# Performance work log

Measured on AMD Instinct MI355X. Metric: run time of the kernel, lower is better.

Reference implementation:

```python
import jax, jax.numpy as jnp
import numpy as np

B, T, K, H = 4, 2048, 1024, 16
D = K // H

def setup_inputs() -> dict:
    key = jax.random.key(0)
    kx, kq, kk, kv = jax.random.split(key, 4)
    s = 1.0 / np.sqrt(K)
    return {
        "x": jax.random.normal(kx, (B, T, K), dtype=jnp.float32),
        "Wq": jax.random.normal(kq, (K, K), dtype=jnp.float32) * s,
        "Wk": jax.random.normal(kk, (K, K), dtype=jnp.float32) * s,
        "Wv": jax.random.normal(kv, (K, K), dtype=jnp.float32) * s,
    }

def reference(x, Wq, Wk, Wv):
    b, t, k = x.shape
    h, d = H, K // H
    # projections -> (b, h, t, d)
    q = (x @ Wq.T).reshape(b, t, h, d).transpose(0, 2, 1, 3)
    ke = (x @ Wk.T).reshape(b, t, h, d).transpose(0, 2, 1, 3)
    v = (x @ Wv.T).reshape(b, t, h, d).transpose(0, 2, 1, 3)
    scale = d ** (-0.25)  # applied to both q and k, as in the original
    scores = jnp.einsum('bhqd,bhkd->bhqk', q * scale, ke * scale)
    causal = jnp.triu(jnp.ones((t, t), dtype=bool), k=1)
    scores = jnp.where(causal, -jnp.inf, scores)
    attn = jax.nn.softmax(scores, axis=-1)
    out = jnp.einsum('bhqk,bhkd->bhqd', attn, v)
    return out.transpose(0, 2, 1, 3).reshape(b, t, k)
```

## Files before the change

kernel.cpp:

```cpp
#include <hip/hip_runtime.h>
#include <hip/hip_bf16.h>
#include <math.h>

#define B_   4
#define T_   2048
#define KDIM 1024
#define H_   16
#define D_   64
#define BH_  (B_*H_)
#define M_   (B_*T_)
#define NKT  (KDIM/64)

typedef __bf16 bf16;
typedef __bf16 bf16x8 __attribute__((ext_vector_type(8)));
typedef __bf16 bf16x4 __attribute__((ext_vector_type(4)));
typedef float  f32x4  __attribute__((ext_vector_type(4)));
typedef float  f32x16 __attribute__((ext_vector_type(16)));
typedef unsigned int u32;
typedef u32 u32x4 __attribute__((ext_vector_type(4)));

static __device__ __forceinline__ f32x4 mfma16(bf16x8 a, bf16x8 b, f32x4 c) {
    return __builtin_amdgcn_mfma_f32_16x16x32_bf16(a, b, c, 0, 0, 0);
}
static __device__ __forceinline__ f32x16 mfma32(bf16x8 a, bf16x8 b, f32x16 c) {
    return __builtin_amdgcn_mfma_f32_32x32x16_bf16(a, b, c, 0, 0, 0);
}
static __device__ __forceinline__ float exp2_fast(float x) {
    float r; asm("v_exp_f32 %0, %1" : "=v"(r) : "v"(x)); return r;
}

__global__ void cvt_all(const float* __restrict__ x,  const float* __restrict__ Wq,
                        const float* __restrict__ Wk, const float* __restrict__ Wv,
                        bf16* __restrict__ dst) {
    int i = blockIdx.x * blockDim.x + threadIdx.x;
    const int NX = M_*KDIM/4, NW = KDIM*KDIM/4;
    const float* src;
    int j;
    if (i < NX)                { src = x;  j = i; }
    else if (i < NX + NW)      { src = Wq; j = i - NX; }
    else if (i < NX + 2*NW)    { src = Wk; j = i - NX - NW; }
    else                       { src = Wv; j = i - NX - 2*NW; }
    float4 v = reinterpret_cast<const float4*>(src)[j];
    bf16x4 o;
    o.x = (bf16)v.x; o.y = (bf16)v.y; o.z = (bf16)v.z; o.w = (bf16)v.w;
    reinterpret_cast<bf16x4*>(dst)[i] = o;
}

__global__ __launch_bounds__(512) void proj_gemm256(
    const bf16* __restrict__ xb, const bf16* __restrict__ Wflat,
    bf16* __restrict__ Qb, bf16* __restrict__ Kb, bf16* __restrict__ Vtb)
{
    __shared__ __align__(16) char As[3*32768];
    __shared__ __align__(16) char Bs[3*16384];

    const int tid  = threadIdx.x;
    const int wid  = tid >> 6;
    const int lane = tid & 63;
    const int l15  = lane & 15, l4 = lane >> 4;
    const int wavem = wid >> 1, waven = wid & 1;

    const int orig = blockIdx.x;
    const int xcd  = orig & 7;
    const int idx  = orig >> 3;
    const int mblk = xcd * 4 + (idx & 3);
    const int nblk = idx >> 2;
    const int row0 = mblk * 256, col0 = nblk * 128;

    const bf16* asrc[4];
#pragma unroll
    for (int q = 0; q < 4; ++q) {
        int c   = q*512 + tid;
        int rr  = c >> 3;
        int cb  = (c & 7) * 16;
        int cbs = cb ^ ((rr & 7) << 4);
        asrc[q] = xb + (size_t)(row0 + rr)*KDIM + (cbs >> 1);
    }
    const bf16* bsrc[2];
#pragma unroll
    for (int q = 0; q < 2; ++q) {
        int c   = q*512 + tid;
        int rr  = c >> 3;
        int cb  = (c & 7) * 16;
        int cbs = cb ^ ((rr & 7) << 4);
        bsrc[q] = Wflat + (size_t)(col0 + rr)*KDIM + (cbs >> 1);
    }

    auto stage = [&](int kt, int buf) {
        const int k0 = kt * 64;
        char* Ab = As + buf*32768;
        char* Bb = Bs + buf*16384;
#pragma unroll
        for (int q = 0; q < 4; ++q) {
            char* la = Ab + (q*512 + wid*64)*16;
            __builtin_amdgcn_global_load_lds(
                (const __attribute__((address_space(1))) void*)(asrc[q] + k0),
                (__attribute__((address_space(3))) void*)la, 16, 0, 0);
        }
#pragma unroll
        for (int q = 0; q < 2; ++q) {
            char* lb = Bb + (q*512 + wid*64)*16;
            __builtin_amdgcn_global_load_lds(
                (const __attribute__((address_space(1))) void*)(bsrc[q] + k0),
                (__attribute__((address_space(3))) void*)lb, 16, 0, 0);
        }
    };

    f32x4 acc[4][4] = {};

    const int sw    = (l15 & 7) << 4;
    const int arow  = (wavem*64 + l15) * 128;
    const int brow  = (waven*64 + l15) * 128;

    stage(0, 0);
    stage(1, 1);
    asm volatile("s_waitcnt vmcnt(6)" ::: "memory");
    __builtin_amdgcn_sched_barrier(0);
    __builtin_amdgcn_s_barrier();

#pragma unroll
    for (int t = 0; t < NKT; ++t) {
        const int bt = t % 3;
        const int b2 = (t + 2) % 3;
        if (t + 2 < NKT) stage(t + 2, b2);

        const char* Ap = As + bt*32768;
        const char* Bp = Bs + bt*16384;
        bf16x8 af[2][4], bfr[2][4];
#pragma unroll
        for (int kk = 0; kk < 2; ++kk) {
            const int cbk = (kk*64 + l4*16) ^ sw;
#pragma unroll
            for (int m = 0; m < 4; ++m)
                af[kk][m] = *reinterpret_cast<const bf16x8*>(Ap + arow + m*2048 + cbk);
#pragma unroll
            for (int n = 0; n < 4; ++n)
                bfr[kk][n] = *reinterpret_cast<const bf16x8*>(Bp + brow + n*2048 + cbk);
        }
        __builtin_amdgcn_s_setprio(1);
#pragma unroll
        for (int kk = 0; kk < 2; ++kk)
#pragma unroll
            for (int m = 0; m < 4; ++m)
#pragma unroll
                for (int n = 0; n < 4; ++n)
                    acc[m][n] = mfma16(af[kk][m], bfr[kk][n], acc[m][n]);
        __builtin_amdgcn_s_setprio(0);

        if (t < NKT - 1) {
            if (t + 2 < NKT) {
                asm volatile("s_waitcnt vmcnt(6)" ::: "memory");
            } else {
                asm volatile("s_waitcnt vmcnt(0)" ::: "memory");
            }
            __builtin_amdgcn_sched_barrier(0);
            __builtin_amdgcn_s_barrier();
        }
    }

#pragma unroll
    for (int m = 0; m < 4; ++m)
#pragma unroll
        for (int n = 0; n < 4; ++n)
#pragma unroll
            for (int r = 0; r < 4; ++r) {
                int gi = row0 + wavem*64 + m*16 + l4*4 + r;
                int gj = col0 + waven*64 + n*16 + l15;
                int wz  = gj >> 10;
                int gjw = gj & 1023;
                float v = acc[m][n][r];
                if (wz == 0) v *= 0.18033688011112042f;
                bf16 o = (bf16)v;
                int bb = gi >> 11, tt = gi & (T_-1);
                int hh = gjw >> 6, dd = gjw & (D_-1);
                size_t bh = (size_t)bb*H_ + hh;
                if (wz == 0)      Qb [(bh*T_ + tt)*D_ + dd] = o;
                else if (wz == 1) Kb [(bh*T_ + tt)*D_ + dd] = o;
                else              Vtb[(bh*D_ + dd)*T_ + tt] = o;
            }
}

__global__ __launch_bounds__(256) void flash_attn3(
    const bf16* __restrict__ Qb, const bf16* __restrict__ Kb,
    const bf16* __restrict__ Vtb, float* __restrict__ out)
{
    __shared__ __align__(16) char Ksm[8192];
    __shared__ __align__(16) char Vsm[8192];

    const int tid  = threadIdx.x;
    const int wid  = tid >> 6;
    const int lane = tid & 63;
    const int l31  = lane & 31;
    const int hi   = lane >> 5;

    const int orig = blockIdx.x;
    const int wg   = (orig & 7) * 128 + (orig >> 3);
    const int bh   = wg >> 4;
    const int qblk = (15 - (wg & 15)) * 128;
    const int q0   = qblk + wid * 32;
    const int q_abs = q0 + l31;

    const bf16* qp = Qb + ((size_t)bh*T_ + q_abs)*D_ + hi*8;
    bf16x8 qf[4];
#pragma unroll
    for (int j = 0; j < 4; ++j)
        qf[j] = *reinterpret_cast<const bf16x8*>(qp + j*16);

    const bf16* kbase = Kb  + (size_t)bh*T_*D_;
    const bf16* vbase = Vtb + (size_t)bh*D_*T_;

    f32x16 o0 = {}; f32x16 o1 = {};
    float lsum = 0.f;

    const int my_nt  = (q0 + 31) >> 6;
    const int blk_nt = qblk/64 + 1;
    const int tmaskb = q_abs - 4*hi;

    const int r0 = tid >> 3,          r1 = (tid + 256) >> 3;
    const int e0 = (tid & 7) * 8,     e1 = e0;
    const u32 lds0 = (u32)((r0*128 + e0*2) ^ ((r0 & 7) << 4));
    const u32 lds1 = (u32)((r1*128 + e1*2) ^ ((r1 & 7) << 4));

    u32x4 kr0, kr1, vr0, vr1;
    auto issue = [&](int nt) {
        kr0 = *reinterpret_cast<const u32x4*>(kbase + ((size_t)(nt*64 + r0))*D_ + e0);
        kr1 = *reinterpret_cast<const u32x4*>(kbase + ((size_t)(nt*64 + r1))*D_ + e1);
        vr0 = *reinterpret_cast<const u32x4*>(vbase + (size_t)r0*T_ + nt*64 + e0);
        vr1 = *reinterpret_cast<const u32x4*>(vbase + (size_t)r1*T_ + nt*64 + e1);
    };
    issue(0);

    auto subtile = [&](int s, int kvb_abs, bool maskit, bf16x8& pA, bf16x8& pB) {
        f32x16 sacc = {};
        const int row = s*32 + l31;
        const int swk = (row & 7) << 4;
#pragma unroll
        for (int j = 0; j < 4; ++j) {
            bf16x8 kf = *reinterpret_cast<const bf16x8*>(Ksm + ((row*128 + j*32 + hi*16) ^ swk));
            sacc = mfma32(kf, qf[j], sacc);
        }
        const int tlim = tmaskb - kvb_abs;
        float p[16];
#pragma unroll
        for (int r = 0; r < 16; ++r) {
            const int crow0 = (r & 3) + 8*(r >> 2);
            float sv = sacc[r];
            if (maskit) sv = (crow0 > tlim) ? -INFINITY : sv;
            p[r] = exp2_fast(sv);
        }
        {
            float a0 = p[0]+p[1],   a1 = p[2]+p[3],   a2 = p[4]+p[5],   a3 = p[6]+p[7];
            float a4 = p[8]+p[9],   a5 = p[10]+p[11], a6 = p[12]+p[13], a7 = p[14]+p[15];
            lsum += ((a0+a1) + (a2+a3)) + ((a4+a5) + (a6+a7));
        }
        u32 w[8];
#pragma unroll
        for (int i = 0; i < 8; ++i) {
            u32 wv;
            asm("v_cvt_pk_bf16_f32 %0, %1, %2" : "=v"(wv) : "v"(p[2*i]), "v"(p[2*i+1]));
            w[i] = wv;
        }
        u32 a0w = w[0], a2w = w[2];
        asm("v_permlane32_swap_b32 %0, %1" : "+v"(a0w), "+v"(a2w));
        u32 a1w = w[1], a3w = w[3];
        asm("v_permlane32_swap_b32 %0, %1" : "+v"(a1w), "+v"(a3w));
        u32 b0w = w[4], b2w = w[6];
        asm("v_permlane32_swap_b32 %0, %1" : "+v"(b0w), "+v"(b2w));
        u32 b1w = w[5], b3w = w[7];
        asm("v_permlane32_swap_b32 %0, %1" : "+v"(b1w), "+v"(b3w));
        u32x4 A0 = {a0w, a1w, a2w, a3w};
        u32x4 A1 = {b0w, b1w, b2w, b3w};
        pA = __builtin_bit_cast(bf16x8, A0);
        pB = __builtin_bit_cast(bf16x8, A1);
    };

    auto pv = [&](int ks, bf16x8 pf) {
        const int swv = (l31 & 7) << 4;
        const int colb = ks*32 + hi*16;
        bf16x8 v0 = *reinterpret_cast<const bf16x8*>(Vsm + ((l31*128 + colb) ^ swv));
        bf16x8 v1 = *reinterpret_cast<const bf16x8*>(Vsm + (((32 + l31)*128 + colb) ^ swv));
        o0 = mfma32(v0, pf, o0);
        o1 = mfma32(v1, pf, o1);
    };

    for (int nt = 0; nt <= blk_nt; ++nt) {
        __syncthreads();
        *reinterpret_cast<u32x4*>(Ksm + lds0) = kr0;
        *reinterpret_cast<u32x4*>(Ksm + lds1) = kr1;
        *reinterpret_cast<u32x4*>(Vsm + lds0) = vr0;
        *reinterpret_cast<u32x4*>(Vsm + lds1) = vr1;
        __syncthreads();
        if (nt < blk_nt) issue(nt + 1);

        if (nt <= my_nt) {
            const bool partial = (nt == my_nt);
            const int  nsub = (!partial || (q0 & 32)) ? 2 : 1;
            bf16x8 pA, pB;
            subtile(0, nt*64, partial, pA, pB);
            pv(0, pA);
            pv(1, pB);
            if (nsub == 2) {
                subtile(1, nt*64 + 32, partial, pA, pB);
                pv(2, pA);
                pv(3, pB);
            }
        }
    }

    lsum += __shfl_xor(lsum, 32);
    const float inv = 1.0f / lsum;
    const int bb = bh >> 4, hh = bh & 15;
    float* orow = out + ((size_t)bb*T_ + q_abs)*KDIM + hh*64 + hi*4;
#pragma unroll
    for (int g = 0; g < 4; ++g) {
        f32x4 v0, v1;
#pragma unroll
        for (int j = 0; j < 4; ++j) { v0[j] = o0[g*4+j]*inv; v1[j] = o1[g*4+j]*inv; }
        *reinterpret_cast<f32x4*>(orow + g*8)      = v0;
        *reinterpret_cast<f32x4*>(orow + 32 + g*8) = v1;
    }
}

extern "C" void kernel_launch(void* const* d_in, const int* in_sizes, int n_in,
                              void* d_out, int out_size, void* d_ws, size_t ws_size,
                              hipStream_t stream) {
    (void)in_sizes; (void)n_in; (void)out_size; (void)ws_size;
    const float* x  = (const float*)d_in[0];
    const float* Wq = (const float*)d_in[1];
    const float* Wk = (const float*)d_in[2];
    const float* Wv = (const float*)d_in[3];
    float* out = (float*)d_out;

    bf16* xb  = (bf16*)d_ws;
    bf16* Wb  = xb + (size_t)M_*KDIM;
    bf16* Qb  = Wb + (size_t)3*KDIM*KDIM;
    bf16* Kb  = Qb + (size_t)M_*KDIM;
    bf16* Vtb = Kb + (size_t)M_*KDIM;

    const int n4 = (M_*KDIM + 3*KDIM*KDIM) / 4;
    cvt_all<<<(n4 + 255)/256, 256, 0, stream>>>(x, Wq, Wk, Wv, xb);

    proj_gemm256<<<dim3(768), 512, 0, stream>>>(xb, Wb, Qb, Kb, Vtb);
    flash_attn3<<<dim3(BH_*16), 256, 0, stream>>>(Qb, Kb, Vtb, out);
}
```

Baseline: 153.6 us.

## Enlarge projection GEMM tile to 256x256 with four-phase interleaved loads

The QKV projection GEMM moves from a 256x128 tile with a triple-buffered stage to a 256x256 tile with double buffering. Each k-step is split into four compute phases, and the global-to-LDS loads for the next k-tile are spread across those phases with explicit barriers and waitcnts. The intent is more arithmetic per byte loaded and better overlap of loads with MFMA work. In exchange, the grid halves to 384 blocks on 256 CUs, which leaves some CUs with a second wave of blocks. It also doubles the accumulator registers and adds more barriers per k-step.

```diff
diff --git a/kernel.cpp b/kernel.cpp
--- a/kernel.cpp
+++ b/kernel.cpp
@@ -46,125 +46,120 @@
     reinterpret_cast<bf16x4*>(dst)[i] = o;
 }
 
-__global__ __launch_bounds__(512) void proj_gemm256(
+__global__ __launch_bounds__(512) void proj_gemm8p(
     const bf16* __restrict__ xb, const bf16* __restrict__ Wflat,
     bf16* __restrict__ Qb, bf16* __restrict__ Kb, bf16* __restrict__ Vtb)
 {
-    __shared__ __align__(16) char As[3*32768];
-    __shared__ __align__(16) char Bs[3*16384];
+    __shared__ __align__(16) char As[2*32768];
+    __shared__ __align__(16) char Bs[2*32768];
 
     const int tid  = threadIdx.x;
     const int wid  = tid >> 6;
     const int lane = tid & 63;
     const int l15  = lane & 15, l4 = lane >> 4;
-    const int wavem = wid >> 1, waven = wid & 1;
+    const int wm   = wid >> 2;
+    const int wn   = wid & 3;
 
     const int orig = blockIdx.x;
     const int xcd  = orig & 7;
     const int idx  = orig >> 3;
     const int mblk = xcd * 4 + (idx & 3);
     const int nblk = idx >> 2;
-    const int row0 = mblk * 256, col0 = nblk * 128;
-
-    const bf16* asrc[4];
-#pragma unroll
-    for (int q = 0; q < 4; ++q) {
-        int c   = q*512 + tid;
-        int rr  = c >> 3;
-        int cb  = (c & 7) * 16;
-        int cbs = cb ^ ((rr & 7) << 4);
-        asrc[q] = xb + (size_t)(row0 + rr)*KDIM + (cbs >> 1);
+    const int row0 = mblk * 256, col0 = nblk * 256;
+
+    const int srow  = tid >> 3;
+    const int scolb = (tid & 7) * 16;
+    const int scbs  = scolb ^ ((srow & 7) << 4);
+    const bf16* aS[4]; const bf16* bS[4];
+#pragma unroll
+    for (int c = 0; c < 4; ++c) {
+        aS[c] = xb    + (size_t)(row0 + c*64 + srow)*KDIM + (scbs >> 1);
+        bS[c] = Wflat + (size_t)(col0 + c*64 + srow)*KDIM + (scbs >> 1);
     }
-    const bf16* bsrc[2];
-#pragma unroll
-    for (int q = 0; q < 2; ++q) {
-        int c   = q*512 + tid;
-        int rr  = c >> 3;
-        int cb  = (c & 7) * 16;
-        int cbs = cb ^ ((rr & 7) << 4);
-        bsrc[q] = Wflat + (size_t)(col0 + rr)*KDIM + (cbs >> 1);
-    }
-
-    auto stage = [&](int kt, int buf) {
-        const int k0 = kt * 64;
-        char* Ab = As + buf*32768;
-        char* Bb = Bs + buf*16384;
-#pragma unroll
-        for (int q = 0; q < 4; ++q) {
-            char* la = Ab + (q*512 + wid*64)*16;
-            __builtin_amdgcn_global_load_lds(
-                (const __attribute__((address_space(1))) void*)(asrc[q] + k0),
-                (__attribute__((address_space(3))) void*)la, 16, 0, 0);
-        }
-#pragma unroll
-        for (int q = 0; q < 2; ++q) {
-            char* lb = Bb + (q*512 + wid*64)*16;
-            __builtin_amdgcn_global_load_lds(
-                (const __attribute__((address_space(1))) void*)(bsrc[q] + k0),
-                (__attribute__((address_space(3))) void*)lb, 16, 0, 0);
-        }
-    };
-
-    f32x4 acc[4][4] = {};
-
-    const int sw    = (l15 & 7) << 4;
-    const int arow  = (wavem*64 + l15) * 128;
-    const int brow  = (waven*64 + l15) * 128;
-
-    stage(0, 0);
-    stage(1, 1);
-    asm volatile("s_waitcnt vmcnt(6)" ::: "memory");
+
+    auto stA = [&](int kt, int c) {
+        if (kt >= NKT) return;
+        char* d = As + ((kt & 1)*32768 + c*8192 + wid*1024);
+        __builtin_amdgcn_global_load_lds(
+            (const __attribute__((address_space(1))) void*)(aS[c] + kt*64),
+            (__attribute__((address_space(3))) void*)d, 16, 0, 0);
+    };
+    auto stB = [&](int kt, int c) {
+        if (kt >= NKT) return;
+        char* d = Bs + ((kt & 1)*32768 + c*8192 + wid*1024);
+        __builtin_amdgcn_global_load_lds(
+            (const __attribute__((address_space(1))) void*)(bS[c] + kt*64),
+            (__attribute__((address_space(3))) void*)d, 16, 0, 0);
+    };
+
+    f32x4 acc[8][4] = {};
+    const int sw = (l15 & 7) << 4;
+
+#define PHASE(MQ, NQ, STAGES, WAITS) do {                                              \
+    bf16x8 af_[2][4]; bf16x8 bf_[2][2];                                                \
+    _Pragma("unroll")                                                                  \
+    for (int kk = 0; kk < 2; ++kk) {                                                   \
+        const int cbk = (kk*64 + l4*16) ^ sw;                                          \
+        _Pragma("unroll")                                                              \
+        for (int m = 0; m < 4; ++m)                                                    \
+            af_[kk][m] = *reinterpret_cast<const bf16x8*>(                             \
+                Ap + (wm*128 + (MQ)*64 + m*16 + l15)*128 + cbk);                       \
+        _Pragma("unroll")                                                              \
+        for (int n = 0; n < 2; ++n)                                                    \
+            bf_[kk][n] = *reinterpret_cast<const bf16x8*>(                             \
+                Bp + (wn*64 + (NQ)*32 + n*16 + l15)*128 + cbk);                        \
+    }                                                                                  \
+    STAGES;                                                                            \
+    WAITS;                                                                             \
+    __builtin_amdgcn_s_barrier();                                                      \
+    __builtin_amdgcn_sched_barrier(0);                                                 \
+    asm volatile("s_waitcnt lgkmcnt(0)" ::: "memory");                                 \
+    __builtin_amdgcn_sched_barrier(0);                                                 \
+    __builtin_amdgcn_s_setprio(1);                                                     \
+    _Pragma("unroll")                                                                  \
+    for (int kk = 0; kk < 2; ++kk)                                                     \
+        _Pragma("unroll")                                                              \
+        for (int m = 0; m < 4; ++m)                                                    \
+            _Pragma("unroll")                                                          \
+            for (int n = 0; n < 2; ++n)                                                \
+                acc[(MQ)*4+m][(NQ)*2+n] =                                              \
+                    mfma16(af_[kk][m], bf_[kk][n], acc[(MQ)*4+m][(NQ)*2+n]);           \
+    __builtin_amdgcn_s_setprio(0);                                                     \
+    __builtin_amdgcn_s_barrier();                                                      \
+    __builtin_amdgcn_sched_barrier(0);                                                 \
+} while (0)
+
+#pragma unroll
+    for (int c = 0; c < 4; ++c) { stA(0, c); stB(0, c); }
+    asm volatile("s_waitcnt vmcnt(0)" ::: "memory");
     __builtin_amdgcn_sched_barrier(0);
     __builtin_amdgcn_s_barrier();
 
-#pragma unroll
     for (int t = 0; t < NKT; ++t) {
-        const int bt = t % 3;
-        const int b2 = (t + 2) % 3;
-        if (t + 2 < NKT) stage(t + 2, b2);
-
-        const char* Ap = As + bt*32768;
-        const char* Bp = Bs + bt*16384;
-        bf16x8 af[2][4], bfr[2][4];
-#pragma unroll
-        for (int kk = 0; kk < 2; ++kk) {
-            const int cbk = (kk*64 + l4*16) ^ sw;
-#pragma unroll
-            for (int m = 0; m < 4; ++m)
-                af[kk][m] = *reinterpret_cast<const bf16x8*>(Ap + arow + m*2048 + cbk);
-#pragma unroll
-            for (int n = 0; n < 4; ++n)
-                bfr[kk][n] = *reinterpret_cast<const bf16x8*>(Bp + brow + n*2048 + cbk);
-        }
-        __builtin_amdgcn_s_setprio(1);
-#pragma unroll
-        for (int kk = 0; kk < 2; ++kk)
-#pragma unroll
-            for (int m = 0; m < 4; ++m)
-#pragma unroll
-                for (int n = 0; n < 4; ++n)
-                    acc[m][n] = mfma16(af[kk][m], bfr[kk][n], acc[m][n]);
-        __builtin_amdgcn_s_setprio(0);
-
-        if (t < NKT - 1) {
-            if (t + 2 < NKT) {
-                asm volatile("s_waitcnt vmcnt(6)" ::: "memory");
-            } else {
-                asm volatile("s_waitcnt vmcnt(0)" ::: "memory");
-            }
-            __builtin_amdgcn_sched_barrier(0);
-            __builtin_amdgcn_s_barrier();
-        }
+        const char* Ap = As + (t & 1)*32768;
+        const char* Bp = Bs + (t & 1)*32768;
+        const bool more = (t < NKT - 1);
+
+        PHASE(0, 0, { stA(t+1, 0); stA(t+1, 2); }, (void)0);
+        PHASE(0, 1, { stB(t+1, 0); stB(t+1, 1); },
+              { if (more) { asm volatile("s_waitcnt vmcnt(4)" ::: "memory"); }
+                else      { asm volatile("s_waitcnt vmcnt(0)" ::: "memory"); }
+                __builtin_amdgcn_sched_barrier(0); });
+        PHASE(1, 0, { stB(t+1, 2); stB(t+1, 3); }, (void)0);
+        PHASE(1, 1, { stA(t+1, 1); stA(t+1, 3); },
+              { if (more) { asm volatile("s_waitcnt vmcnt(2)" ::: "memory");
+                            __builtin_amdgcn_sched_barrier(0); } });
     }
-
-#pragma unroll
-    for (int m = 0; m < 4; ++m)
+#undef PHASE
+
+#pragma unroll
+    for (int m = 0; m < 8; ++m)
 #pragma unroll
         for (int n = 0; n < 4; ++n)
 #pragma unroll
             for (int r = 0; r < 4; ++r) {
-                int gi = row0 + wavem*64 + m*16 + l4*4 + r;
-                int gj = col0 + waven*64 + n*16 + l15;
+                int gi = row0 + wm*128 + m*16 + l4*4 + r;
+                int gj = col0 + wn*64  + n*16 + l15;
                 int wz  = gj >> 10;
                 int gjw = gj & 1023;
                 float v = acc[m][n][r];
@@ -216,16 +211,16 @@
     const int tmaskb = q_abs - 4*hi;
 
     const int r0 = tid >> 3,          r1 = (tid + 256) >> 3;
-    const int e0 = (tid & 7) * 8,     e1 = e0;
+    const int e0 = (tid & 7) * 8;
     const u32 lds0 = (u32)((r0*128 + e0*2) ^ ((r0 & 7) << 4));
-    const u32 lds1 = (u32)((r1*128 + e1*2) ^ ((r1 & 7) << 4));
+    const u32 lds1 = (u32)((r1*128 + e0*2) ^ ((r1 & 7) << 4));
 
     u32x4 kr0, kr1, vr0, vr1;
     auto issue = [&](int nt) {
         kr0 = *reinterpret_cast<const u32x4*>(kbase + ((size_t)(nt*64 + r0))*D_ + e0);
-        kr1 = *reinterpret_cast<const u32x4*>(kbase + ((size_t)(nt*64 + r1))*D_ + e1);
+        kr1 = *reinterpret_cast<const u32x4*>(kbase + ((size_t)(nt*64 + r1))*D_ + e0);
         vr0 = *reinterpret_cast<const u32x4*>(vbase + (size_t)r0*T_ + nt*64 + e0);
-        vr1 = *reinterpret_cast<const u32x4*>(vbase + (size_t)r1*T_ + nt*64 + e1);
+        vr1 = *reinterpret_cast<const u32x4*>(vbase + (size_t)r1*T_ + nt*64 + e0);
     };
     issue(0);
 
@@ -339,6 +334,6 @@
     const int n4 = (M_*KDIM + 3*KDIM*KDIM) / 4;
     cvt_all<<<(n4 + 255)/256, 256, 0, stream>>>(x, Wq, Wk, Wv, xb);
 
-    proj_gemm256<<<dim3(768), 512, 0, stream>>>(xb, Wb, Qb, Kb, Vtb);
+    proj_gemm8p<<<dim3(384), 512, 0, stream>>>(xb, Wb, Qb, Kb, Vtb);
     flash_attn3<<<dim3(BH_*16), 256, 0, stream>>>(Qb, Kb, Vtb, out);
 }
```

Measured after the change: 178.3 us. +16.1%, slower.

## Replace triple-buffered 256x128 projection GEMM with single-buffered 128x128 tiles

Applied to the files above, without the earlier changes.

The projection GEMM goes from 256x128 tiles with 512 threads and a three-stage LDS pipeline to 128x128 tiles with 256 threads and one LDS buffer, synchronised with syncthreads and a full vmcnt(0) wait each k-step. The grid doubles to 1536 blocks and LDS per block shrinks a lot, which could allow more resident blocks and hide latency through occupancy rather than software pipelining. The cost is that loads no longer overlap the MFMA work inside a block, each tile is reused less, and the priority hints are removed. The attention kernel only has a redundant variable removed.

```diff
diff --git a/kernel.cpp b/kernel.cpp
--- a/kernel.cpp
+++ b/kernel.cpp
@@ -46,114 +46,77 @@
     reinterpret_cast<bf16x4*>(dst)[i] = o;
 }
 
-__global__ __launch_bounds__(512) void proj_gemm256(
+__global__ __launch_bounds__(256) void proj_gemm97(
     const bf16* __restrict__ xb, const bf16* __restrict__ Wflat,
     bf16* __restrict__ Qb, bf16* __restrict__ Kb, bf16* __restrict__ Vtb)
 {
-    __shared__ __align__(16) char As[3*32768];
-    __shared__ __align__(16) char Bs[3*16384];
+    __shared__ __align__(16) char Asm[128*128];
+    __shared__ __align__(16) char Bsm[128*128];
 
     const int tid  = threadIdx.x;
     const int wid  = tid >> 6;
     const int lane = tid & 63;
     const int l15  = lane & 15, l4 = lane >> 4;
-    const int wavem = wid >> 1, waven = wid & 1;
+    const int wr = wid >> 1, wc = wid & 1;
 
     const int orig = blockIdx.x;
     const int xcd  = orig & 7;
     const int idx  = orig >> 3;
-    const int mblk = xcd * 4 + (idx & 3);
-    const int nblk = idx >> 2;
-    const int row0 = mblk * 256, col0 = nblk * 128;
-
-    const bf16* asrc[4];
+    const int mblk = xcd * 8 + (idx & 7);
+    const int nblk = idx >> 3;
+    const int row0 = mblk * 128, col0 = nblk * 128;
+
+    const bf16* aS[4]; const bf16* bS[4];
 #pragma unroll
     for (int q = 0; q < 4; ++q) {
-        int c   = q*512 + tid;
+        int c   = q*256 + tid;
         int rr  = c >> 3;
         int cb  = (c & 7) * 16;
         int cbs = cb ^ ((rr & 7) << 4);
-        asrc[q] = xb + (size_t)(row0 + rr)*KDIM + (cbs >> 1);
+        aS[q] = xb    + (size_t)(row0 + rr)*KDIM + (cbs >> 1);
+        bS[q] = Wflat + (size_t)(col0 + rr)*KDIM + (cbs >> 1);
     }
-    const bf16* bsrc[2];
-#pragma unroll
-    for (int q = 0; q < 2; ++q) {
-        int c   = q*512 + tid;
-        int rr  = c >> 3;
-        int cb  = (c & 7) * 16;
-        int cbs = cb ^ ((rr & 7) << 4);
-        bsrc[q] = Wflat + (size_t)(col0 + rr)*KDIM + (cbs >> 1);
-    }
-
-    auto stage = [&](int kt, int buf) {
+
+    f32x4 acc[4][4] = {};
+    const int sw   = (l15 & 7) << 4;
+    const int arow = (wr*64 + l15) * 128;
+    const int brow = (wc*64 + l15) * 128;
+
+    for (int kt = 0; kt < NKT; ++kt) {
         const int k0 = kt * 64;
-        char* Ab = As + buf*32768;
-        char* Bb = Bs + buf*16384;
+        __syncthreads();
 #pragma unroll
         for (int q = 0; q < 4; ++q) {
-            char* la = Ab + (q*512 + wid*64)*16;
+            char* la = Asm + (q*256 + wid*64)*16;
             __builtin_amdgcn_global_load_lds(
-                (const __attribute__((address_space(1))) void*)(asrc[q] + k0),
+                (const __attribute__((address_space(1))) void*)(aS[q] + k0),
                 (__attribute__((address_space(3))) void*)la, 16, 0, 0);
         }
 #pragma unroll
-        for (int q = 0; q < 2; ++q) {
-            char* lb = Bb + (q*512 + wid*64)*16;
+        for (int q = 0; q < 4; ++q) {
+            char* lb = Bsm + (q*256 + wid*64)*16;
             __builtin_amdgcn_global_load_lds(
-                (const __attribute__((address_space(1))) void*)(bsrc[q] + k0),
+                (const __attribute__((address_space(1))) void*)(bS[q] + k0),
                 (__attribute__((address_space(3))) void*)lb, 16, 0, 0);
         }
-    };
-
-    f32x4 acc[4][4] = {};
-
-    const int sw    = (l15 & 7) << 4;
-    const int arow  = (wavem*64 + l15) * 128;
-    const int brow  = (waven*64 + l15) * 128;
-
-    stage(0, 0);
-    stage(1, 1);
-    asm volatile("s_waitcnt vmcnt(6)" ::: "memory");
-    __builtin_amdgcn_sched_barrier(0);
-    __builtin_amdgcn_s_barrier();
-
-#pragma unroll
-    for (int t = 0; t < NKT; ++t) {
-        const int bt = t % 3;
-        const int b2 = (t + 2) % 3;
-        if (t + 2 < NKT) stage(t + 2, b2);
-
-        const char* Ap = As + bt*32768;
-        const char* Bp = Bs + bt*16384;
-        bf16x8 af[2][4], bfr[2][4];
+        asm volatile("s_waitcnt vmcnt(0)" ::: "memory");
+        __syncthreads();
+
 #pragma unroll
         for (int kk = 0; kk < 2; ++kk) {
             const int cbk = (kk*64 + l4*16) ^ sw;
+            bf16x8 af[4], bfr[4];
 #pragma unroll
             for (int m = 0; m < 4; ++m)
-                af[kk][m] = *reinterpret_cast<const bf16x8*>(Ap + arow + m*2048 + cbk);
+                af[m] = *reinterpret_cast<const bf16x8*>(Asm + arow + m*2048 + cbk);
 #pragma unroll
             for (int n = 0; n < 4; ++n)
-                bfr[kk][n] = *reinterpret_cast<const bf16x8*>(Bp + brow + n*2048 + cbk);
-        }
-        __builtin_amdgcn_s_setprio(1);
-#pragma unroll
-        for (int kk = 0; kk < 2; ++kk)
+                bfr[n] = *reinterpret_cast<const bf16x8*>(Bsm + brow + n*2048 + cbk);
 #pragma unroll
             for (int m = 0; m < 4; ++m)
 #pragma unroll
                 for (int n = 0; n < 4; ++n)
-                    acc[m][n] = mfma16(af[kk][m], bfr[kk][n], acc[m][n]);
-        __builtin_amdgcn_s_setprio(0);
-
-        if (t < NKT - 1) {
-            if (t + 2 < NKT) {
-                asm volatile("s_waitcnt vmcnt(6)" ::: "memory");
-            } else {
-                asm volatile("s_waitcnt vmcnt(0)" ::: "memory");
-            }
-            __builtin_amdgcn_sched_barrier(0);
-            __builtin_amdgcn_s_barrier();
+                    acc[m][n] = mfma16(af[m], bfr[n], acc[m][n]);
         }
     }
 
@@ -163,8 +126,8 @@
         for (int n = 0; n < 4; ++n)
 #pragma unroll
             for (int r = 0; r < 4; ++r) {
-                int gi = row0 + wavem*64 + m*16 + l4*4 + r;
-                int gj = col0 + waven*64 + n*16 + l15;
+                int gi = row0 + wr*64 + m*16 + l4*4 + r;
+                int gj = col0 + wc*64 + n*16 + l15;
                 int wz  = gj >> 10;
                 int gjw = gj & 1023;
                 float v = acc[m][n][r];
@@ -216,16 +179,16 @@
     const int tmaskb = q_abs - 4*hi;
 
     const int r0 = tid >> 3,          r1 = (tid + 256) >> 3;
-    const int e0 = (tid & 7) * 8,     e1 = e0;
+    const int e0 = (tid & 7) * 8;
     const u32 lds0 = (u32)((r0*128 + e0*2) ^ ((r0 & 7) << 4));
-    const u32 lds1 = (u32)((r1*128 + e1*2) ^ ((r1 & 7) << 4));
+    const u32 lds1 = (u32)((r1*128 + e0*2) ^ ((r1 & 7) << 4));
 
     u32x4 kr0, kr1, vr0, vr1;
     auto issue = [&](int nt) {
         kr0 = *reinterpret_cast<const u32x4*>(kbase + ((size_t)(nt*64 + r0))*D_ + e0);
-        kr1 = *reinterpret_cast<const u32x4*>(kbase + ((size_t)(nt*64 + r1))*D_ + e1);
+        kr1 = *reinterpret_cast<const u32x4*>(kbase + ((size_t)(nt*64 + r1))*D_ + e0);
         vr0 = *reinterpret_cast<const u32x4*>(vbase + (size_t)r0*T_ + nt*64 + e0);
-        vr1 = *reinterpret_cast<const u32x4*>(vbase + (size_t)r1*T_ + nt*64 + e1);
+        vr1 = *reinterpret_cast<const u32x4*>(vbase + (size_t)r1*T_ + nt*64 + e0);
     };
     issue(0);
 
@@ -339,6 +302,6 @@
     const int n4 = (M_*KDIM + 3*KDIM*KDIM) / 4;
     cvt_all<<<(n4 + 255)/256, 256, 0, stream>>>(x, Wq, Wk, Wv, xb);
 
-    proj_gemm256<<<dim3(768), 512, 0, stream>>>(xb, Wb, Qb, Kb, Vtb);
+    proj_gemm97<<<dim3(1536), 256, 0, stream>>>(xb, Wb, Qb, Kb, Vtb);
     flash_attn3<<<dim3(BH_*16), 256, 0, stream>>>(Qb, Kb, Vtb, out);
 }
```

Result: slower. 163.1 us (+6.2%).
